# Performance work log

Measured on AMD Instinct MI355X. Metric: run time of the kernel, lower is better.

## Reference

```python
import jax, jax.numpy as jnp
import numpy as np

N_HEADS = 16
N_KV_HEADS = 4
HEAD_DIM = 128


def apply_rotary_emb(x, cos, sin):
    # x: [B, S, H, D]; cos/sin: [S, D//2]
    xr = x[..., 0::2]
    xi = x[..., 1::2]
    c = cos[None, :, None, :]
    s = sin[None, :, None, :]
    out_r = xr * c - xi * s
    out_i = xr * s + xi * c
    # interleave back: [..., D//2, 2] -> [..., D]
    return jnp.stack([out_r, out_i], axis=-1).reshape(x.shape)


def setup_inputs() -> dict:
    key = jax.random.key(0)
    ks = jax.random.split(key, 7)
    B, S, D = 4, 2048, 2048
    x = jax.random.normal(ks[0], (B, S, D), dtype=jnp.float32)
    # realistic rotary tables
    inv_freq = 1.0 / (10000.0 ** (jnp.arange(0, HEAD_DIM, 2, dtype=jnp.float32) / HEAD_DIM))
    t = jnp.arange(S, dtype=jnp.float32)
    freqs = jnp.outer(t, inv_freq)  # [S, D/2]
    freqs_cos = jnp.cos(freqs)
    freqs_sin = jnp.sin(freqs)
    sc = 0.02
    wq = jax.random.normal(ks[1], (D, N_HEADS * HEAD_DIM), dtype=jnp.float32) * sc
    wk = jax.random.normal(ks[2], (D, N_KV_HEADS * HEAD_DIM), dtype=jnp.float32) * sc
    wv = jax.random.normal(ks[3], (D, N_KV_HEADS * HEAD_DIM), dtype=jnp.float32) * sc
    wo = jax.random.normal(ks[4], (N_HEADS * HEAD_DIM, D), dtype=jnp.float32) * sc
    return {"x": x, "freqs_cos": freqs_cos, "freqs_sin": freqs_sin,
            "wq": wq, "wk": wk, "wv": wv, "wo": wo}


def reference(x, freqs_cos, freqs_sin, wq, wk, wv, wo):
    B, S, D = x.shape
    n_rep = N_HEADS // N_KV_HEADS
    xq = (x @ wq).reshape(B, S, N_HEADS, HEAD_DIM)
    xk = (x @ wk).reshape(B, S, N_KV_HEADS, HEAD_DIM)
    xv = (x @ wv).reshape(B, S, N_KV_HEADS, HEAD_DIM)
    xq = apply_rotary_emb(xq, freqs_cos, freqs_sin)
    xk = apply_rotary_emb(xk, freqs_cos, freqs_sin)
    # repeat_kv (GQA): [B,S,Hkv,D] -> [B,S,Hkv*n_rep,D]
    xk = jnp.repeat(xk, n_rep, axis=2)
    xv = jnp.repeat(xv, n_rep, axis=2)
    # [B,H,S,D]
    q = xq.transpose(0, 2, 1, 3)
    k = xk.transpose(0, 2, 1, 3)
    v = xv.transpose(0, 2, 1, 3)
    scores = jnp.einsum('bhqd,bhkd->bhqk', q, k) / jnp.sqrt(jnp.float32(HEAD_DIM))
    causal = jnp.triu(jnp.ones((S, S), dtype=bool), k=1)
    scores = jnp.where(causal[None, None], -jnp.inf, scores)
    probs = jax.nn.softmax(scores, axis=-1)
    out = jnp.einsum('bhqk,bhkd->bhqd', probs, v)
    out = out.transpose(0, 2, 1, 3).reshape(B, S, N_HEADS * HEAD_DIM)
    return out @ wo
```

## Files before the change

### kernel.cpp

```cpp
#include <hip/hip_runtime.h>
#include <stdint.h>
#include <stddef.h>

#define B_ 4
#define S_ 2048
#define D_ 2048
#define NH 16
#define NKV 4
#define HD 128
#define QKV_N 3072
#define ROWS (B_*S_)

typedef unsigned short u16;
typedef __attribute__((ext_vector_type(8))) unsigned short u16x8;
typedef __attribute__((ext_vector_type(8))) __bf16 bf16x8;
typedef __attribute__((ext_vector_type(4))) float f32x4;

__device__ __forceinline__ u16 f2bf(float f) {
  unsigned u = __builtin_bit_cast(unsigned, f);
  return (u16)((u + 0x7fffu + ((u >> 16) & 1u)) >> 16);
}
__device__ __forceinline__ float bf2f(u16 h) {
  return __builtin_bit_cast(float, (unsigned)h << 16);
}
__device__ __forceinline__ f32x4 mfma16(u16x8 a, u16x8 b, f32x4 c) {
  return __builtin_amdgcn_mfma_f32_16x16x32_bf16(
      __builtin_bit_cast(bf16x8, a), __builtin_bit_cast(bf16x8, b), c, 0, 0, 0);
}
__device__ __forceinline__ void gld16(const void* g, void* l) {
  __builtin_amdgcn_global_load_lds(
      (const __attribute__((address_space(1))) void*)g,
      (__attribute__((address_space(3))) void*)l, 16, 0, 0);
}

__global__ __launch_bounds__(256) void k_cast_x(const float* __restrict__ x, u16* __restrict__ xb) {
  int i = blockIdx.x * 256 + threadIdx.x;
  float4 v = ((const float4*)x)[i];
  union { u16 u[4]; uint2 p; } o;
  o.u[0] = f2bf(v.x); o.u[1] = f2bf(v.y); o.u[2] = f2bf(v.z); o.u[3] = f2bf(v.w);
  ((uint2*)xb)[i] = o.p;
}

__global__ __launch_bounds__(256) void k_wt(const float* __restrict__ w, u16* __restrict__ wt, int K, int N) {
  __shared__ float tile[32][33];
  int kb = blockIdx.y * 32, nb = blockIdx.x * 32;
  int tx = threadIdx.x, ty = threadIdx.y;
#pragma unroll
  for (int j = 0; j < 32; j += 8)
    tile[ty + j][tx] = w[(size_t)(kb + ty + j) * N + nb + tx];
  __syncthreads();
#pragma unroll
  for (int j = 0; j < 32; j += 8)
    wt[(size_t)(nb + ty + j) * K + kb + tx] = f2bf(tile[tx][ty + j]);
}


#define STG_A(KK, SS) do {                                                   \
    gld16(Ag + (size_t)r0 * 2048 + (KK) + coff, As + (SS) * 8192 + stl0);    \
    gld16(Ag + (size_t)(r0 + 128) * 2048 + (KK) + coff,                      \
          As + (SS) * 8192 + stl1);                                          \
  } while (0)
#define STG_B(KK, SS) do {                                                   \
    gld16(Bg + (size_t)r0 * 2048 + (KK) + coff, Bs + (SS) * 8192 + stl0);    \
    gld16(Bg + (size_t)(r0 + 128) * 2048 + (KK) + coff,                      \
          Bs + (SS) * 8192 + stl1);                                          \
  } while (0)

#define PHASE(RS, MB, RB, SS, SK, SA, VM) do {                               \
    if (SA) STG_A(SK, SS); else STG_B(SK, SS);                               \
    const u16* Ap_ = As + (RS) * 8192;                                       \
    _Pragma("unroll") for (int i_ = 0; i_ < 4; ++i_)                         \
      af[i_] = *(const u16x8*)(Ap_ + arow0 + ((MB) + i_) * 512);             \
    if (RB) {                                                                \
      const u16* Bp_ = Bs + (RS) * 8192;                                     \
      _Pragma("unroll") for (int i_ = 0; i_ < 4; ++i_)                       \
        bf[i_] = *(const u16x8*)(Bp_ + brow0 + i_ * 512);                    \
    }                                                                        \
    __builtin_amdgcn_s_setprio(1);                                           \
    _Pragma("unroll") for (int i_ = 0; i_ < 4; ++i_)                         \
      _Pragma("unroll") for (int n_ = 0; n_ < 4; ++n_)                       \
        acc[(MB) + i_][n_] = mfma16(af[i_], bf[n_], acc[(MB) + i_][n_]);     \
    __builtin_amdgcn_s_setprio(0);                                           \
    if (VM) asm volatile("s_waitcnt vmcnt(8)" ::: "memory");                 \
    asm volatile("s_barrier" ::: "memory");                                  \
  } while (0)

template<int NT, bool F32OUT>
__global__ __launch_bounds__(512, 2) void k_gemm(const u16* __restrict__ A, const u16* __restrict__ Bt,
                                                 void* __restrict__ C) {
  __shared__ u16 As[4 * 8192];
  __shared__ u16 Bs[4 * 8192];
  int id = blockIdx.x;
  int nwg = gridDim.x;
  id = (id & 7) * (nwg >> 3) + (id >> 3);
  const int gx = NT / 256;
  int mb = (id / gx) * 256, nb = (id % gx) * 256;

  int t = threadIdx.x;
  int l = t & 63, L16 = l & 15, quad = l >> 4;
  int w = t >> 6, wm = w >> 2, wn = w & 3;
  const int schunk = 8 * (quad ^ (L16 & 3));
  const int arow0 = (wm * 128 + L16) * 32 + schunk;
  const int brow0 = (wn * 64 + L16) * 32 + schunk;
  const int r0 = t >> 2;
  const int coff = 8 * ((t & 3) ^ (r0 & 3));
  const int stl0 = (t & 448) * 8, stl1 = stl0 + 4096;

  const u16* Ag = A + (size_t)mb * 2048;
  const u16* Bg = Bt + (size_t)nb * 2048;
  u16x8 af[4], bf[4];
  f32x4 acc[8][4] = {};

  STG_A(0, 0);  STG_B(0, 0);
  STG_A(32, 1); STG_B(32, 1);
  STG_A(64, 2); STG_B(64, 2);
  asm volatile("s_waitcnt vmcnt(8)" ::: "memory");
  asm volatile("s_barrier" ::: "memory");

#pragma unroll 1
  for (int tp = 0; tp < 16; ++tp) {
    int t0 = tp * 2;
    int ka1 = ((t0 + 1) & 31) * 64 + 32;
    int ka2 = ((t0 + 2) & 31) * 64;
    int kb1 = ((t0 + 2) & 31) * 64 + 32;
    int kb2 = ((t0 + 3) & 31) * 64;
    PHASE(0, 0, true,  3, ka1, true,  false);
    PHASE(0, 4, false, 3, ka1, false, true);
    PHASE(1, 0, true,  0, ka2, true,  false);
    PHASE(1, 4, false, 0, ka2, false, true);
    PHASE(2, 0, true,  1, kb1, true,  false);
    PHASE(2, 4, false, 1, kb1, false, true);
    PHASE(3, 0, true,  2, kb2, true,  false);
    PHASE(3, 4, false, 2, kb2, false, true);
  }
  asm volatile("s_waitcnt vmcnt(0)" ::: "memory");

#pragma unroll
  for (int m = 0; m < 8; ++m)
#pragma unroll
    for (int n = 0; n < 4; ++n)
#pragma unroll
      for (int r = 0; r < 4; ++r) {
        int row = mb + wm * 128 + m * 16 + quad * 4 + r;
        int col = nb + wn * 64 + n * 16 + L16;
        if constexpr (F32OUT)
          ((float*)C)[(size_t)row * NT + col] = acc[m][n][r];
        else
          ((u16*)C)[(size_t)row * NT + col] = f2bf(acc[m][n][r]);
      }
}

__global__ __launch_bounds__(256) void k_rope(const u16* __restrict__ qkv, const float* __restrict__ fc,
                                              const float* __restrict__ fs, u16* __restrict__ Q,
                                              u16* __restrict__ Kk) {
  const float SC = 0.1275174214f;
  int row = blockIdx.x;
  int b = row >> 11, s = row & 2047;
  int t = threadIdx.x;
#pragma unroll
  for (int j = 0; j < 5; ++j) {
    int p = t + j * 256;
    int i = p & 63;
    float c = fc[s * 64 + i], sn = fs[s * 64 + i];
    if (p < 1024) {
      int h = p >> 6;
      unsigned pr = *(const unsigned*)(qkv + (size_t)row * QKV_N + h * 128 + 2 * i);
      float xr = bf2f((u16)(pr & 0xffff)), xi = bf2f((u16)(pr >> 16));
      size_t o = (((size_t)(b * NH + h) * S_) + s) * HD + 2 * i;
      unsigned out = (unsigned)f2bf((xr * c - xi * sn) * SC) |
                     ((unsigned)f2bf((xr * sn + xi * c) * SC) << 16);
      *(unsigned*)(Q + o) = out;
    } else {
      int kh = (p - 1024) >> 6;
      unsigned pr = *(const unsigned*)(qkv + (size_t)row * QKV_N + 2048 + kh * 128 + 2 * i);
      float xr = bf2f((u16)(pr & 0xffff)), xi = bf2f((u16)(pr >> 16));
      size_t o = (((size_t)(b * NKV + kh) * S_) + s) * HD + 2 * i;
      unsigned out = (unsigned)f2bf(xr * c - xi * sn) | ((unsigned)f2bf(xr * sn + xi * c) << 16);
      *(unsigned*)(Kk + o) = out;
    }
  }
}

__global__ __launch_bounds__(256) void k_vt(const u16* __restrict__ qkv, u16* __restrict__ Vt) {
  __shared__ u16 tile[64 * 128];
  int blk = blockIdx.x;
  int sb = blk & 31, kh = (blk >> 5) & 3, b = blk >> 7;
  int t = threadIdx.x;
  int s0 = sb * 64;
#pragma unroll
  for (int i = 0; i < 4; ++i) {
    int lin = i * 256 + t;
    int row = lin >> 4, c = lin & 15;
    u16x8 v = *(const u16x8*)(qkv + (size_t)(b * S_ + s0 + row) * QKV_N + 2560 + kh * HD + c * 8);
    *(u16x8*)(tile + row * 128 + ((c ^ (row & 15)) * 8)) = v;
  }
  __syncthreads();
#pragma unroll
  for (int i = 0; i < 2; ++i) {
    int u = i * 256 + t;
    int p = u >> 3, o = u & 7;
    u16 lo[8], hi[8];
#pragma unroll
    for (int j = 0; j < 8; ++j) {
      int s = o * 8 + j;
      int cs = (p >> 2) ^ (s & 15);
      unsigned v = *(const unsigned*)(tile + s * 128 + cs * 8 + (p & 3) * 2);
      lo[j] = (u16)(v & 0xffff); hi[j] = (u16)(v >> 16);
    }
    size_t ob = ((size_t)(b * NKV + kh) * HD + 2 * p) * S_ + s0 + o * 8;
    *(u16x8*)(Vt + ob)      = *(u16x8*)lo;
    *(u16x8*)(Vt + ob + S_) = *(u16x8*)hi;
  }
}

__global__ __launch_bounds__(256) void k_attn(const u16* __restrict__ Q, const u16* __restrict__ Kg,
                                              const u16* __restrict__ Vt, u16* __restrict__ O) {
  int bx = blockIdx.x;
  int bh = bx >> 3, pr = bx & 7;
  int b = bh >> 4, h = bh & 15, kh = h >> 2;
  int t = threadIdx.x;
  int w = t >> 6, l = t & 63, L = l & 15, quad = l >> 4;

  __shared__ u16 Ks[64 * 128];
  __shared__ u16 Vs[128 * 64];
  __shared__ u16 Ps[4][32 * 72];
  u16* Pw = &Ps[w][0];

  const u16* Qh = Q  + ((size_t)(b * NH  + h ) * S_) * HD;
  const u16* Kh = Kg + ((size_t)(b * NKV + kh) * S_) * HD;
  const u16* Vh = Vt + ((size_t)(b * NKV + kh) * HD) * S_;

  u16x8 ones;
#pragma unroll
  for (int i = 0; i < 8; ++i) ones[i] = 0x3F80;

  int koff[4], voff[2];
#pragma unroll
  for (int kk = 0; kk < 4; ++kk) koff[kk] = 128 * L + 8 * ((4 * kk + quad) ^ (L & 7));
#pragma unroll
  for (int kc = 0; kc < 2; ++kc) voff[kc] = 64 * L + 8 * ((4 * kc + quad) ^ (L & 7));
  const int pread  = 72 * L + 8 * quad;
  const int pwrite = 72 * L + 4 * quad;

  int kgo[4], vgo[4], klo[4], vlo[4];
#pragma unroll
  for (int i = 0; i < 4; ++i) {
    int lin = i * 256 + t;
    int row = lin >> 4, c = lin & 15;
    kgo[i] = row * HD + ((c ^ (row & 7)) * 8);
    int d = lin >> 3, c2 = lin & 7;
    vgo[i] = d * S_ + ((c2 ^ (d & 7)) * 8);
    klo[i] = (i * 256 + (t & 192)) * 8;
    vlo[i] = (i * 256 + (t & 192)) * 8;
  }

#pragma unroll 1
  for (int half = 0; half < 2; ++half) {
    int qb = half ? (15 - pr) : pr;
    int q0 = qb * 128 + w * 32;

    u16x8 qf[2][4];
#pragma unroll
    for (int m = 0; m < 2; ++m)
#pragma unroll
      for (int kk = 0; kk < 4; ++kk)
        qf[m][kk] = *(const u16x8*)(Qh + (size_t)(q0 + m * 16 + L) * HD + kk * 32 + quad * 8);

    f32x4 acc[2][9] = {};
    int ktiles = 2 * qb + 2;
#pragma unroll 1
    for (int kt = 0; kt < ktiles; ++kt) {
      int kbase = kt * 64;
      __syncthreads();
      const u16* Kt = Kh + (size_t)kbase * HD;
      const u16* Vg = Vh + kbase;
#pragma unroll
      for (int i = 0; i < 4; ++i) gld16(Kt + kgo[i], Ks + klo[i]);
#pragma unroll
      for (int i = 0; i < 4; ++i) gld16(Vg + vgo[i], Vs + vlo[i]);
      __syncthreads();
      if (kbase > q0 + 31) continue;

      bool needMask = (kbase + 63 > q0);
#pragma unroll
      for (int n = 0; n < 4; ++n) {
        f32x4 s0v = {}, s1v = {};
#pragma unroll
        for (int kk = 0; kk < 4; ++kk) {
          u16x8 kf = *(const u16x8*)(Ks + koff[kk] + 2048 * n);
          s0v = mfma16(kf, qf[0][kk], s0v);
          s1v = mfma16(kf, qf[1][kk], s1v);
        }
#pragma unroll
        for (int m = 0; m < 2; ++m) {
          f32x4 sv = m ? s1v : s0v;
          int qrow = q0 + m * 16 + L;
          unsigned eu[4];
#pragma unroll
          for (int r = 0; r < 4; ++r) {
            float e = exp2f(sv[r]);
            if (needMask) {
              int key = kbase + n * 16 + quad * 4 + r;
              e = (key <= qrow) ? e : 0.0f;
            }
            eu[r] = __builtin_bit_cast(unsigned, e);
          }
          uint2 pk;
          pk.x = __builtin_amdgcn_perm(eu[1], eu[0], 0x07060302u);
          pk.y = __builtin_amdgcn_perm(eu[3], eu[2], 0x07060302u);
          *(uint2*)(Pw + pwrite + 1152 * m + 16 * n) = pk;
        }
      }
#pragma unroll
      for (int kc = 0; kc < 2; ++kc) {
        u16x8 pf0 = *(const u16x8*)(Pw + pread + 32 * kc);
        u16x8 pf1 = *(const u16x8*)(Pw + pread + 1152 + 32 * kc);
#pragma unroll
        for (int nt = 0; nt < 8; ++nt) {
          u16x8 vf = *(const u16x8*)(Vs + voff[kc] + 1024 * nt);
          acc[0][nt] = mfma16(pf0, vf, acc[0][nt]);
          acc[1][nt] = mfma16(pf1, vf, acc[1][nt]);
        }
        acc[0][8] = mfma16(pf0, ones, acc[0][8]);
        acc[1][8] = mfma16(pf1, ones, acc[1][8]);
      }
    }
#pragma unroll
    for (int m = 0; m < 2; ++m)
#pragma unroll
      for (int r = 0; r < 4; ++r) {
        float inv = 1.0f / acc[m][8][r];
        int qrow = q0 + m * 16 + quad * 4 + r;
#pragma unroll
        for (int nt = 0; nt < 8; ++nt) {
          int col = h * HD + nt * 16 + L;
          O[(size_t)(b * S_ + qrow) * D_ + col] = f2bf(acc[m][nt][r] * inv);
        }
      }
  }
}

extern "C" void kernel_launch(void* const* d_in, const int* in_sizes, int n_in,
                              void* d_out, int out_size, void* d_ws, size_t ws_size,
                              hipStream_t stream) {
  const float* x  = (const float*)d_in[0];
  const float* fc = (const float*)d_in[1];
  const float* fs = (const float*)d_in[2];
  const float* wq = (const float*)d_in[3];
  const float* wk = (const float*)d_in[4];
  const float* wv = (const float*)d_in[5];
  const float* wo = (const float*)d_in[6];
  float* out = (float*)d_out;

  u16* p = (u16*)d_ws;
  u16* xb    = p; p += (size_t)ROWS * D_;
  u16* wqkvT = p; p += (size_t)QKV_N * D_;
  u16* woT   = p; p += (size_t)D_ * D_;
  u16* qkv   = p; p += (size_t)ROWS * QKV_N;
  u16* Qr    = p; p += (size_t)ROWS * (NH * HD);
  u16* Kr    = p; p += (size_t)ROWS * (NKV * HD);
  u16* Vtr   = p; p += (size_t)ROWS * (NKV * HD);
  u16* AO    = p; p += (size_t)ROWS * D_;

  k_cast_x<<<dim3(ROWS * D_ / 1024), dim3(256), 0, stream>>>(x, xb);
  k_wt<<<dim3(64, 64), dim3(32, 8), 0, stream>>>(wq, wqkvT, 2048, 2048);
  k_wt<<<dim3(16, 64), dim3(32, 8), 0, stream>>>(wk, wqkvT + (size_t)2048 * 2048, 2048, 512);
  k_wt<<<dim3(16, 64), dim3(32, 8), 0, stream>>>(wv, wqkvT + (size_t)2560 * 2048, 2048, 512);
  k_wt<<<dim3(64, 64), dim3(32, 8), 0, stream>>>(wo, woT, 2048, 2048);
  k_gemm<QKV_N, false><<<dim3((QKV_N / 256) * (ROWS / 256)), dim3(512), 0, stream>>>(xb, wqkvT, qkv);
  k_rope<<<dim3(ROWS), dim3(256), 0, stream>>>(qkv, fc, fs, Qr, Kr);
  k_vt<<<dim3(B_ * NKV * (S_ / 64)), dim3(256), 0, stream>>>(qkv, Vtr);
  k_attn<<<dim3(64 * 8), dim3(256), 0, stream>>>(Qr, Kr, Vtr, AO);
  k_gemm<D_, true><<<dim3((D_ / 256) * (ROWS / 256)), dim3(512), 0, stream>>>(AO, woT, out);
}
```

Measured before the change: 466.2 us.

## Restructure GEMM pipeline: LDS reads before global stage, shallower prefetch, new swizzle

Reorders each phase of the bf16 GEMM main loop so the LDS fragment reads are issued before the next global-to-LDS stage, then adds an extra barrier, an lgkmcnt wait and scheduling barriers around the MFMA block. Prefetch depth drops from three stages to two (vmcnt 8 to 4), and the loop becomes a 32-iteration loop with computed stage indices, unrolled by 2. The LDS swizzle changes to XOR with bits 1-2 of the row instead of bits 0-1, meant to cut bank conflicts. The extra barrier per phase and the shallower prefetch may expose more global-load latency.

```diff
diff --git a/kernel.cpp b/kernel.cpp
--- a/kernel.cpp
+++ b/kernel.cpp
@@ -67,7 +67,6 @@
   } while (0)
 
 #define PHASE(RS, MB, RB, SS, SK, SA, VM) do {                               \
-    if (SA) STG_A(SK, SS); else STG_B(SK, SS);                               \
     const u16* Ap_ = As + (RS) * 8192;                                       \
     _Pragma("unroll") for (int i_ = 0; i_ < 4; ++i_)                         \
       af[i_] = *(const u16x8*)(Ap_ + arow0 + ((MB) + i_) * 512);             \
@@ -76,12 +75,17 @@
       _Pragma("unroll") for (int i_ = 0; i_ < 4; ++i_)                       \
         bf[i_] = *(const u16x8*)(Bp_ + brow0 + i_ * 512);                    \
     }                                                                        \
+    if (SA) STG_A(SK, SS); else STG_B(SK, SS);                               \
+    asm volatile("s_barrier" ::: "memory");                                  \
+    asm volatile("s_waitcnt lgkmcnt(0)" ::: "memory");                       \
+    __builtin_amdgcn_sched_barrier(0);                                       \
     __builtin_amdgcn_s_setprio(1);                                           \
     _Pragma("unroll") for (int i_ = 0; i_ < 4; ++i_)                         \
       _Pragma("unroll") for (int n_ = 0; n_ < 4; ++n_)                       \
         acc[(MB) + i_][n_] = mfma16(af[i_], bf[n_], acc[(MB) + i_][n_]);     \
     __builtin_amdgcn_s_setprio(0);                                           \
-    if (VM) asm volatile("s_waitcnt vmcnt(8)" ::: "memory");                 \
+    __builtin_amdgcn_sched_barrier(0);                                       \
+    if (VM) asm volatile("s_waitcnt vmcnt(4)" ::: "memory");                 \
     asm volatile("s_barrier" ::: "memory");                                  \
   } while (0)
 
@@ -99,11 +103,11 @@
   int t = threadIdx.x;
   int l = t & 63, L16 = l & 15, quad = l >> 4;
   int w = t >> 6, wm = w >> 2, wn = w & 3;
-  const int schunk = 8 * (quad ^ (L16 & 3));
+  const int schunk = 8 * (quad ^ ((L16 >> 1) & 3));
   const int arow0 = (wm * 128 + L16) * 32 + schunk;
   const int brow0 = (wn * 64 + L16) * 32 + schunk;
   const int r0 = t >> 2;
-  const int coff = 8 * ((t & 3) ^ (r0 & 3));
+  const int coff = 8 * ((t & 3) ^ ((r0 >> 1) & 3));
   const int stl0 = (t & 448) * 8, stl1 = stl0 + 4096;
 
   const u16* Ag = A + (size_t)mb * 2048;
@@ -113,25 +117,18 @@
 
   STG_A(0, 0);  STG_B(0, 0);
   STG_A(32, 1); STG_B(32, 1);
-  STG_A(64, 2); STG_B(64, 2);
-  asm volatile("s_waitcnt vmcnt(8)" ::: "memory");
+  asm volatile("s_waitcnt vmcnt(4)" ::: "memory");
   asm volatile("s_barrier" ::: "memory");
 
-#pragma unroll 1
-  for (int tp = 0; tp < 16; ++tp) {
-    int t0 = tp * 2;
-    int ka1 = ((t0 + 1) & 31) * 64 + 32;
-    int ka2 = ((t0 + 2) & 31) * 64;
-    int kb1 = ((t0 + 2) & 31) * 64 + 32;
-    int kb2 = ((t0 + 3) & 31) * 64;
-    PHASE(0, 0, true,  3, ka1, true,  false);
-    PHASE(0, 4, false, 3, ka1, false, true);
-    PHASE(1, 0, true,  0, ka2, true,  false);
-    PHASE(1, 4, false, 0, ka2, false, true);
-    PHASE(2, 0, true,  1, kb1, true,  false);
-    PHASE(2, 4, false, 1, kb1, false, true);
-    PHASE(3, 0, true,  2, kb2, true,  false);
-    PHASE(3, 4, false, 2, kb2, false, true);
+#pragma unroll 2
+  for (int tt = 0; tt < 32; ++tt) {
+    int rs0 = (2 * tt) & 3,     rs1 = (2 * tt + 1) & 3;
+    int ws0 = (2 * tt + 2) & 3, ws1 = (2 * tt + 3) & 3;
+    int kn = ((tt + 1) & 31) * 64;
+    PHASE(rs0, 0, true,  ws0, kn,      true,  false);
+    PHASE(rs0, 4, false, ws0, kn,      false, true);
+    PHASE(rs1, 0, true,  ws1, kn + 32, true,  false);
+    PHASE(rs1, 4, false, ws1, kn + 32, false, true);
   }
   asm volatile("s_waitcnt vmcnt(0)" ::: "memory");
 
```

Result: no change. 458.3 us (-1.7%).
